# Optimization experiments

Hardware: AMD Instinct MI355X
Metric: run time of the kernel (lower is better)

Reference implementation:

```python
import jax, jax.numpy as jnp
import numpy as np

DIM = 128; NH = 4; WS = 7; SS = 3
ZP, HP, WP = 14, 56, 56
NMLP = 512; EPS = 1e-5
N = WS ** 3  # tokens per window (343)


def _ln(x, g, b):
    m = x.mean(-1, keepdims=True)
    v = x.var(-1, keepdims=True)
    return (x - m) / jnp.sqrt(v + EPS) * g + b


def _rel_index():
    # static relative-position index for a cubic (WS,WS,WS) window
    c = np.stack(np.meshgrid(np.arange(WS), np.arange(WS), np.arange(WS), indexing='ij')).reshape(3, -1)
    rel = (c[:, :, None] - c[:, None, :]).transpose(1, 2, 0) + (WS - 1)
    rel[..., 0] *= (2 * WS - 1) ** 2
    rel[..., 1] *= (2 * WS - 1)
    return rel.sum(-1).reshape(-1)  # [N*N]


def _attn_mask():
    # static shifted-window attention mask, [nW, N, N]
    img = np.zeros((ZP, HP, WP), np.float32)
    cnt = 0
    sl = (slice(0, -WS), slice(-WS, -SS), slice(-SS, None))
    for z in sl:
        for h in sl:
            for w in sl:
                img[z, h, w] = cnt
                cnt += 1
    m = img.reshape(ZP // WS, WS, HP // WS, WS, WP // WS, WS)
    m = m.transpose(0, 2, 4, 1, 3, 5).reshape(-1, N)
    d = m[:, None, :] - m[:, :, None]
    return np.where(d != 0, np.float32(-100.0), np.float32(0.0))


_REL_IDX = jnp.asarray(_rel_index())
_MASK = jnp.asarray(_attn_mask())


def setup_inputs() -> dict:
    key = jax.random.key(0)
    ks = jax.random.split(key, 8)
    return {
        'x': jax.random.normal(ks[0], (2, ZP, HP, WP, DIM), jnp.float32),
        'norm1_g': jnp.ones((DIM,), jnp.float32),
        'norm1_b': jnp.zeros((DIM,), jnp.float32),
        'qkv_w': jax.random.normal(ks[1], (DIM, 3 * DIM), jnp.float32) * 0.02,
        'qkv_b': jnp.zeros((3 * DIM,), jnp.float32),
        'rel_table': jax.random.normal(ks[2], ((2 * WS - 1) ** 3, NH), jnp.float32) * 0.02,
        'proj_w': jax.random.normal(ks[3], (DIM, DIM), jnp.float32) * 0.02,
        'proj_b': jnp.zeros((DIM,), jnp.float32),
        'norm2_g': jnp.ones((DIM,), jnp.float32),
        'norm2_b': jnp.zeros((DIM,), jnp.float32),
        'fc1_w': jax.random.normal(ks[4], (DIM, NMLP), jnp.float32) * 0.02,
        'fc1_b': jnp.zeros((NMLP,), jnp.float32),
        'fc2_w': jax.random.normal(ks[5], (NMLP, DIM), jnp.float32) * 0.02,
        'fc2_b': jnp.zeros((DIM,), jnp.float32),
    }


def reference(x, norm1_g, norm1_b, qkv_w, qkv_b, rel_table, proj_w, proj_b,
              norm2_g, norm2_b, fc1_w, fc1_b, fc2_w, fc2_b):
    B, Z, H, W, C = x.shape
    hd = C // NH
    scale = hd ** -0.5
    shortcut = x
    xn = _ln(x, norm1_g, norm1_b)
    # cyclic shift
    xs = jnp.roll(xn, (-SS, -SS, -SS), axis=(1, 2, 3))
    # window partition -> [B*nW, N, C]
    xw = xs.reshape(B, Z // WS, WS, H // WS, WS, W // WS, WS, C)
    xw = xw.transpose(0, 1, 3, 5, 2, 4, 6, 7).reshape(-1, N, C)
    qkv = (xw @ qkv_w + qkv_b).reshape(-1, N, 3, NH, hd).transpose(2, 0, 3, 1, 4)
    q, k, v = qkv[0], qkv[1], qkv[2]  # [Bn, NH, N, hd]
    attn = jnp.einsum('bhnd,bhmd->bhnm', q * scale, k)
    bias = rel_table[_REL_IDX].reshape(N, N, NH).transpose(2, 0, 1)  # [NH, N, N]
    attn = attn + bias[None]
    nW = _MASK.shape[0]
    attn = attn.reshape(B, nW, NH, N, N) + _MASK[None, :, None]
    attn = jax.nn.softmax(attn.reshape(-1, NH, N, N), axis=-1)
    out = jnp.einsum('bhnm,bhmd->bhnd', attn, v)
    out = out.transpose(0, 2, 1, 3).reshape(-1, N, C)
    out = out @ proj_w + proj_b
    # window reverse -> [B, Z, H, W, C]
    out = out.reshape(B, Z // WS, H // WS, W // WS, WS, WS, WS, C)
    out = out.transpose(0, 1, 4, 2, 5, 3, 6, 7).reshape(B, Z, H, W, C)
    out = jnp.roll(out, (SS, SS, SS), axis=(1, 2, 3))
    x1 = shortcut + out
    y = _ln(x1, norm2_g, norm2_b)
    y = jax.nn.gelu(y @ fc1_w + fc1_b, approximate=False) @ fc2_w + fc2_b
    return x1 + y
```

## Files before the change

kernel.cpp:

```cpp
#include <hip/hip_runtime.h>


typedef __attribute__((ext_vector_type(8))) _Float16 half8;
typedef __attribute__((ext_vector_type(4))) _Float16 half4;
typedef __attribute__((ext_vector_type(4))) float floatx4;

#define DEV static __device__ __forceinline__

DEV floatx4 MFMA(half8 a, half8 b, floatx4 c) {
  return __builtin_amdgcn_mfma_f32_16x16x32_f16(a, b, c, 0, 0, 0);
}

DEV float gelu_f(float v) {
  return v / (1.f + __expf(-1.702f * v));
}

DEV void stage_load(half8 pf[8], const _Float16* src, int rst, int tid) {
#pragma unroll
  for (int it = 0; it < 8; ++it) {
    int e = it * 256 + tid;
    int row = e >> 4, seg = e & 15;
    pf[it] = *(const half8*)&src[(size_t)row * rst + seg * 8];
  }
}
DEV void stage_store(_Float16* wb, const half8 pf[8], int tid) {
#pragma unroll
  for (int it = 0; it < 8; ++it) {
    int e = it * 256 + tid;
    int row = e >> 4, seg = e & 15;
    *(half8*)&wb[row * 136 + seg * 8] = pf[it];
  }
}
DEV void stage_tile(_Float16* wb, const _Float16* src, int rst, int tid) {
  half8 pf[8];
  stage_load(pf, src, rst, tid);
  stage_store(wb, pf, tid);
}

__global__ __launch_bounds__(256) void k_prep(
    const float* __restrict__ rel, _Float16* __restrict__ biasH,
    const float* __restrict__ w1, const float* __restrict__ w2,
    const float* __restrict__ wq, const float* __restrict__ wp,
    _Float16* __restrict__ w1h, _Float16* __restrict__ w2h,
    _Float16* __restrict__ wqh, _Float16* __restrict__ wph) {
  int gid = blockIdx.x * 256 + threadIdx.x;
  if (gid < 495616) {
    int reg = gid & 3, ml = (gid >> 2) & 15;
    int t = gid >> 6;
    int rb = t % 88; t /= 88;
    int nt = t % 22; int h = t / 22;
    int row = rb * 4 + reg, col = nt * 16 + ml;
    float val = -30000.f;
    if (row < 343 && col < 343) {
      int lzi = row / 49, ri = row - lzi * 49, lhi = ri / 7, lwi = ri - lhi * 7;
      int lzj = col / 49, rj = col - lzj * 49, lhj = rj / 7, lwj = rj - lhj * 7;
      int idx = (lzi - lzj + 6) * 169 + (lhi - lhj + 6) * 13 + (lwi - lwj + 6);
      val = rel[idx * 4 + h];
    }
    biasH[gid] = (_Float16)val;
    return;
  }
  int i = gid - 495616;
  if (i < 65536) {
    int n = i >> 7, k = i & 127;
    w1h[i] = (_Float16)w1[k * 512 + n];
  } else if (i < 131072) {
    int j = i - 65536; int n = j >> 9, k = j & 511;
    w2h[j] = (_Float16)w2[k * 128 + n];
  } else if (i < 180224) {
    int j = i - 131072; int n = j >> 7, k = j & 127;
    wqh[j] = (_Float16)wq[k * 384 + n];
  } else if (i < 196608) {
    int j = i - 180224; int n = j >> 7, k = j & 127;
    wph[j] = (_Float16)wp[k * 128 + n];
  }
}

__global__ __launch_bounds__(256) void k_ln_qkv(
    const float* __restrict__ x, const float* __restrict__ g1,
    const float* __restrict__ b1, const _Float16* __restrict__ wqh,
    const float* __restrict__ bq, _Float16* __restrict__ qkv) {
  __shared__ __align__(16) _Float16 wb[128 * 136];
  const int tid = threadIdx.x, lane = tid & 63, wid = tid >> 6;
  const int ml = lane & 15, quad = lane >> 4;
  const int task = blockIdx.x * 4 + wid;
  const int w = task / 11, pr = task - (task / 11) * 11;
  const int b_ = w >> 7, r = w & 127;
  const int wz = r >> 6, wh = (r >> 3) & 7, ww = r & 7;

  half8 a0[4], a1[4];
#pragma unroll
  for (int hf = 0; hf < 2; ++hf) {
    int t = pr * 32 + hf * 16 + ml; if (t > 342) t = 342;
    int lz = t / 49, rr = t - lz * 49, lh = rr / 7, lw = rr - lh * 7;
    int oz = wz * 7 + lz + 3; if (oz >= 14) oz -= 14;
    int oh = wh * 7 + lh + 3; if (oh >= 56) oh -= 56;
    int ow = ww * 7 + lw + 3; if (ow >= 56) ow -= 56;
    const float* xp = x + ((((b_ * 14 + oz) * 56 + oh) * 56 + ow) << 7);
    float xv[32];
    float s = 0.f, ss = 0.f;
#pragma unroll
    for (int ks = 0; ks < 4; ++ks) {
      float4 p0 = *(const float4*)(xp + ks * 32 + quad * 8);
      float4 p1 = *(const float4*)(xp + ks * 32 + quad * 8 + 4);
      xv[ks * 8 + 0] = p0.x; xv[ks * 8 + 1] = p0.y; xv[ks * 8 + 2] = p0.z; xv[ks * 8 + 3] = p0.w;
      xv[ks * 8 + 4] = p1.x; xv[ks * 8 + 5] = p1.y; xv[ks * 8 + 6] = p1.z; xv[ks * 8 + 7] = p1.w;
      s += (p0.x + p0.y) + (p0.z + p0.w) + (p1.x + p1.y) + (p1.z + p1.w);
      ss += (p0.x * p0.x + p0.y * p0.y) + (p0.z * p0.z + p0.w * p0.w) +
            (p1.x * p1.x + p1.y * p1.y) + (p1.z * p1.z + p1.w * p1.w);
    }
    s += __shfl_xor(s, 16); s += __shfl_xor(s, 32);
    ss += __shfl_xor(ss, 16); ss += __shfl_xor(ss, 32);
    float mean = s * 0.0078125f;
    float rstd = rsqrtf(ss * 0.0078125f - mean * mean + 1e-5f);
#pragma unroll
    for (int ks = 0; ks < 4; ++ks) {
      int k0 = ks * 32 + quad * 8;
      float4 gg0 = *(const float4*)(g1 + k0), gg1 = *(const float4*)(g1 + k0 + 4);
      float4 bb0 = *(const float4*)(b1 + k0), bb1 = *(const float4*)(b1 + k0 + 4);
      half8 a;
      a[0] = (_Float16)((xv[ks * 8 + 0] - mean) * rstd * gg0.x + bb0.x);
      a[1] = (_Float16)((xv[ks * 8 + 1] - mean) * rstd * gg0.y + bb0.y);
      a[2] = (_Float16)((xv[ks * 8 + 2] - mean) * rstd * gg0.z + bb0.z);
      a[3] = (_Float16)((xv[ks * 8 + 3] - mean) * rstd * gg0.w + bb0.w);
      a[4] = (_Float16)((xv[ks * 8 + 4] - mean) * rstd * gg1.x + bb1.x);
      a[5] = (_Float16)((xv[ks * 8 + 5] - mean) * rstd * gg1.y + bb1.y);
      a[6] = (_Float16)((xv[ks * 8 + 6] - mean) * rstd * gg1.z + bb1.z);
      a[7] = (_Float16)((xv[ks * 8 + 7] - mean) * rstd * gg1.w + bb1.w);
      if (hf == 0) a0[ks] = a; else a1[ks] = a;
    }
  }

  for (int c = 0; c < 3; ++c) {
    __syncthreads();
    stage_tile(wb, wqh + (size_t)c * 128 * 128, 128, tid);
    __syncthreads();
    for (int ntl = 0; ntl < 8; ++ntl) {
      floatx4 acc0 = {0.f, 0.f, 0.f, 0.f}, acc1 = {0.f, 0.f, 0.f, 0.f};
#pragma unroll
      for (int ks = 0; ks < 4; ++ks) {
        half8 bb = *(const half8*)&wb[(ntl * 16 + ml) * 136 + ks * 32 + quad * 8];
        acc0 = MFMA(a0[ks], bb, acc0);
        acc1 = MFMA(a1[ks], bb, acc1);
      }
      const int col = c * 128 + ntl * 16 + ml;
      const float qb = bq[col];
#pragma unroll
      for (int reg = 0; reg < 4; ++reg) {
        int t0 = pr * 32 + quad * 4 + reg;
        if (t0 < 343) qkv[((size_t)w * 343 + t0) * 384 + col] = (_Float16)(acc0[reg] + qb);
        int t1 = t0 + 16;
        if (t1 < 343) qkv[((size_t)w * 343 + t1) * 384 + col] = (_Float16)(acc1[reg] + qb);
      }
    }
  }
}

__global__ __launch_bounds__(512)
__attribute__((amdgpu_waves_per_eu(2, 2)))
void k_attn(const _Float16* __restrict__ qkv,
            const _Float16* __restrict__ biasH,
            _Float16* __restrict__ aout) {
  __shared__ __align__(16) _Float16 kl[352 * 40];
  __shared__ __align__(16) _Float16 vt[32 * 360];
  __shared__ __align__(16) _Float16 P[8][16 * 360];
  __shared__ float sums[8][16];
  __shared__ unsigned char region[352];
  const int tid = threadIdx.x;
  const int w = blockIdx.x >> 2, head = blockIdx.x & 3;
  const int r = w & 127;
  const int wz = r >> 6, wh = (r >> 3) & 7, ww = r & 7;
  const bool fz = (wz == 1), fh = (wh == 7), fw = (ww == 7);

  for (int t = tid; t < 352; t += 512) {
    int rg = 255;
    if (t < 343) {
      int lz = t / 49, rr = t - lz * 49, lh = rr / 7, lw = rr - lh * 7;
      int rz = fz ? (lz < 4 ? 1 : 2) : 0;
      int rh2 = fh ? (lh < 4 ? 1 : 2) : 0;
      int rw2 = fw ? (lw < 4 ? 1 : 2) : 0;
      rg = rz * 9 + rh2 * 3 + rw2;
    }
    region[t] = (unsigned char)rg;
  }
  const _Float16* qkvw = qkv + (size_t)w * 343 * 384;
  for (int e = tid; e < 352 * 4; e += 512) {
    int t = e >> 2, d8 = (e & 3) * 8;
    half8 v;
    if (t < 343) {
      v = *(const half8*)&qkvw[t * 384 + 128 + head * 32 + d8];
    } else {
#pragma unroll
      for (int j = 0; j < 8; ++j) v[j] = (_Float16)0.f;
    }
    *(half8*)&kl[t * 40 + d8] = v;
  }
  for (int e = tid; e < 343 * 4; e += 512) {
    int t = e >> 2, d8 = (e & 3) * 8;
    half8 v = *(const half8*)&qkvw[t * 384 + 256 + head * 32 + d8];
#pragma unroll
    for (int j = 0; j < 8; ++j) vt[(d8 + j) * 360 + t] = v[j];
  }
  for (int e = tid; e < 9 * 32; e += 512) {
    int t = 343 + (e >> 5), d = e & 31;
    vt[d * 360 + t] = (_Float16)0.f;
  }
  __syncthreads();

  const int lane = tid & 63, wid = tid >> 6;
  const int ml = lane & 15, quad = lane >> 4;
  _Float16* Pw = &P[wid][0];
  const float scale = 0.17677669529663687f;

  for (int rt = wid; rt < 22; rt += 8) {
    const int row0 = rt * 16;
    int qrow = row0 + ml; if (qrow > 342) qrow = 342;
    half8 aq = *(const half8*)&qkvw[qrow * 384 + head * 32 + quad * 8];
    floatx4 S[22];
#pragma unroll
    for (int nt = 0; nt < 22; ++nt) {
      half8 bk = *(const half8*)&kl[(nt * 16 + ml) * 40 + quad * 8];
      S[nt] = MFMA(aq, bk, (floatx4){0.f, 0.f, 0.f, 0.f});
    }
    int rrow[4];
#pragma unroll
    for (int reg = 0; reg < 4; ++reg) rrow[reg] = region[row0 + quad * 4 + reg];
    const int rb = rt * 4 + quad;
    float sm[4] = {0.f, 0.f, 0.f, 0.f};
#pragma unroll
    for (int nt = 0; nt < 22; ++nt) {
      half4 b4 = *(const half4*)&biasH[((((head * 22 + nt) * 88 + rb) << 4) + ml) * 4];
      int rc = region[nt * 16 + ml];
#pragma unroll
      for (int reg = 0; reg < 4; ++reg) {
        float v = fmaf(S[nt][reg], scale, (float)b4[reg]);
        if (rc != rrow[reg]) v = -30000.f;
        float e = __expf(v);
        sm[reg] += e;
        Pw[(quad * 4 + reg) * 360 + nt * 16 + ml] = (_Float16)e;
      }
    }
#pragma unroll
    for (int d = 1; d < 16; d <<= 1)
#pragma unroll
      for (int reg = 0; reg < 4; ++reg) sm[reg] += __shfl_xor(sm[reg], d, 16);
    if (ml == 0) {
#pragma unroll
      for (int reg = 0; reg < 4; ++reg) sums[wid][quad * 4 + reg] = sm[reg];
    }
    floatx4 o0 = {0.f, 0.f, 0.f, 0.f}, o1 = {0.f, 0.f, 0.f, 0.f};
#pragma unroll
    for (int ks = 0; ks < 11; ++ks) {
      half8 bp = *(const half8*)&Pw[ml * 360 + ks * 32 + quad * 8];
      half8 a0 = *(const half8*)&vt[ml * 360 + ks * 32 + quad * 8];
      half8 a1 = *(const half8*)&vt[(16 + ml) * 360 + ks * 32 + quad * 8];
      o0 = MFMA(a0, bp, o0);
      o1 = MFMA(a1, bp, o1);
    }
    const int orow = row0 + ml;
    if (orow < 343) {
      float inv = 1.f / sums[wid][ml];
      _Float16* op = aout + ((size_t)w * 343 + orow) * 128 + head * 32;
      half4 s0, s1;
#pragma unroll
      for (int reg = 0; reg < 4; ++reg) {
        s0[reg] = (_Float16)(o0[reg] * inv);
        s1[reg] = (_Float16)(o1[reg] * inv);
      }
      *(half4*)&op[quad * 4] = s0;
      *(half4*)&op[16 + quad * 4] = s1;
    }
  }
}

__global__ __launch_bounds__(256)
__attribute__((amdgpu_waves_per_eu(2, 2)))
void k_pm(
    const _Float16* __restrict__ aout, const _Float16* __restrict__ wph,
    const float* __restrict__ bp, const float* __restrict__ x,
    const float* __restrict__ g2, const float* __restrict__ nb2,
    const _Float16* __restrict__ w1h, const float* __restrict__ bfc1,
    const _Float16* __restrict__ w2h, const float* __restrict__ bfc2,
    float* __restrict__ out) {
  __shared__ __align__(16) _Float16 hc[4][32 * 136];
  __shared__ __align__(16) _Float16 wb[128 * 136];
  const int tid = threadIdx.x, lane = tid & 63, wid = tid >> 6;
  const int ml = lane & 15, quad = lane >> 4;
  const int task = blockIdx.x * 4 + wid;
  const int w = task / 11, pr = task - (task / 11) * 11;
  const int b_ = w >> 7, r = w & 127;
  const int wz = r >> 6, wh = (r >> 3) & 7, ww = r & 7;
  const _Float16* ap = aout + (size_t)w * 343 * 128;
  _Float16* hw = &hc[wid][0];

  half8 pf[8];
  stage_load(pf, wph, 128, tid);

  int ra = pr * 32 + ml; if (ra > 342) ra = 342;
  int rbm = pr * 32 + 16 + ml; if (rbm > 342) rbm = 342;
  half8 a0[4], a1[4];
#pragma unroll
  for (int ks = 0; ks < 4; ++ks) {
    a0[ks] = *(const half8*)&ap[ra * 128 + ks * 32 + quad * 8];
    a1[ks] = *(const half8*)&ap[rbm * 128 + ks * 32 + quad * 8];
  }
  int tok[2][4];
#pragma unroll
  for (int mt = 0; mt < 2; ++mt) {
#pragma unroll
    for (int reg = 0; reg < 4; ++reg) {
      int t = pr * 32 + mt * 16 + quad * 4 + reg;
      if (t < 343) {
        int lz = t / 49, rr = t - lz * 49, lh = rr / 7, lw = rr - lh * 7;
        int oz = wz * 7 + lz + 3; if (oz >= 14) oz -= 14;
        int oh = wh * 7 + lh + 3; if (oh >= 56) oh -= 56;
        int ow = ww * 7 + lw + 3; if (ow >= 56) ow -= 56;
        tok[mt][reg] = ((b_ * 14 + oz) * 56 + oh) * 56 + ow;
      } else {
        tok[mt][reg] = -1;
      }
    }
  }
  stage_store(wb, pf, tid);
  __syncthreads();
  stage_load(pf, w1h, 128, tid);

  floatx4 px[8][2];
  for (int nt = 0; nt < 8; ++nt) {
    floatx4 acc0 = {0.f, 0.f, 0.f, 0.f}, acc1 = {0.f, 0.f, 0.f, 0.f};
#pragma unroll
    for (int ks = 0; ks < 4; ++ks) {
      half8 bb = *(const half8*)&wb[(nt * 16 + ml) * 136 + ks * 32 + quad * 8];
      acc0 = MFMA(a0[ks], bb, acc0);
      acc1 = MFMA(a1[ks], bb, acc1);
    }
    const int col = nt * 16 + ml;
    const float pb = bp[col];
#pragma unroll
    for (int reg = 0; reg < 4; ++reg) {
      float xr0 = (tok[0][reg] >= 0) ? x[tok[0][reg] * 128 + col] : 0.f;
      float xr1 = (tok[1][reg] >= 0) ? x[tok[1][reg] * 128 + col] : 0.f;
      px[nt][0][reg] = acc0[reg] + pb + xr0;
      px[nt][1][reg] = acc1[reg] + pb + xr1;
    }
  }

  float mean[2][4], rstd[2][4];
#pragma unroll
  for (int mt = 0; mt < 2; ++mt) {
#pragma unroll
    for (int reg = 0; reg < 4; ++reg) {
      float s = 0.f, ss = 0.f;
#pragma unroll
      for (int nt = 0; nt < 8; ++nt) {
        float v = px[nt][mt][reg];
        s += v; ss += v * v;
      }
#pragma unroll
      for (int d = 1; d < 16; d <<= 1) {
        s += __shfl_xor(s, d, 16);
        ss += __shfl_xor(ss, d, 16);
      }
      float m = s * 0.0078125f;
      mean[mt][reg] = m;
      rstd[mt][reg] = rsqrtf(ss * 0.0078125f - m * m + 1e-5f);
    }
  }

  for (int nt = 0; nt < 8; ++nt) {
    const int col = nt * 16 + ml;
    const float gg = g2[col], bb = nb2[col];
#pragma unroll
    for (int mt = 0; mt < 2; ++mt)
#pragma unroll
      for (int reg = 0; reg < 4; ++reg)
        hw[(mt * 16 + quad * 4 + reg) * 136 + col] =
            (_Float16)((px[nt][mt][reg] - mean[mt][reg]) * rstd[mt][reg] * gg + bb);
  }
  half8 ay[2][4];
#pragma unroll
  for (int mt = 0; mt < 2; ++mt)
#pragma unroll
    for (int ks = 0; ks < 4; ++ks)
      ay[mt][ks] = *(const half8*)&hw[(mt * 16 + ml) * 136 + ks * 32 + quad * 8];

  floatx4 acc2[8][2];
#pragma unroll
  for (int nt = 0; nt < 8; ++nt)
#pragma unroll
    for (int mt = 0; mt < 2; ++mt) acc2[nt][mt] = (floatx4){0.f, 0.f, 0.f, 0.f};

  for (int ch = 0; ch < 4; ++ch) {
    __syncthreads();
    stage_store(wb, pf, tid);
    __syncthreads();
    stage_load(pf, w2h + (size_t)ch * 128, 512, tid);
    for (int nt = 0; nt < 8; ++nt) {
      floatx4 f0 = {0.f, 0.f, 0.f, 0.f}, f1 = {0.f, 0.f, 0.f, 0.f};
#pragma unroll
      for (int ks = 0; ks < 4; ++ks) {
        half8 bb = *(const half8*)&wb[(nt * 16 + ml) * 136 + ks * 32 + quad * 8];
        f0 = MFMA(ay[0][ks], bb, f0);
        f1 = MFMA(ay[1][ks], bb, f1);
      }
      const int col = nt * 16 + ml;
      const float fb = bfc1[ch * 128 + col];
#pragma unroll
      for (int reg = 0; reg < 4; ++reg) {
        hw[(quad * 4 + reg) * 136 + col] = (_Float16)gelu_f(f0[reg] + fb);
        hw[(16 + quad * 4 + reg) * 136 + col] = (_Float16)gelu_f(f1[reg] + fb);
      }
    }
    __syncthreads();
    stage_store(wb, pf, tid);
    __syncthreads();
    if (ch < 3) stage_load(pf, w1h + (size_t)(ch + 1) * 128 * 128, 128, tid);
#pragma unroll
    for (int ks = 0; ks < 4; ++ks) {
      half8 A0 = *(const half8*)&hw[ml * 136 + ks * 32 + quad * 8];
      half8 A1 = *(const half8*)&hw[(16 + ml) * 136 + ks * 32 + quad * 8];
#pragma unroll
      for (int nt = 0; nt < 8; ++nt) {
        half8 bb = *(const half8*)&wb[(nt * 16 + ml) * 136 + ks * 32 + quad * 8];
        acc2[nt][0] = MFMA(A0, bb, acc2[nt][0]);
        acc2[nt][1] = MFMA(A1, bb, acc2[nt][1]);
      }
    }
  }

  for (int nt = 0; nt < 8; ++nt) {
    const int col = nt * 16 + ml;
    const float fb = bfc2[col];
#pragma unroll
    for (int mt = 0; mt < 2; ++mt)
#pragma unroll
      for (int reg = 0; reg < 4; ++reg) {
        if (tok[mt][reg] >= 0)
          out[tok[mt][reg] * 128 + col] = px[nt][mt][reg] + acc2[nt][mt][reg] + fb;
      }
  }
}

extern "C" void kernel_launch(void* const* d_in, const int* in_sizes, int n_in,
                              void* d_out, int out_size, void* d_ws, size_t ws_size,
                              hipStream_t stream) {
  (void)in_sizes; (void)n_in; (void)out_size; (void)ws_size;
  const float* x   = (const float*)d_in[0];
  const float* g1  = (const float*)d_in[1];
  const float* b1  = (const float*)d_in[2];
  const float* wq  = (const float*)d_in[3];
  const float* bq  = (const float*)d_in[4];
  const float* rel = (const float*)d_in[5];
  const float* wp  = (const float*)d_in[6];
  const float* bp  = (const float*)d_in[7];
  const float* g2  = (const float*)d_in[8];
  const float* b2_ = (const float*)d_in[9];
  const float* w1  = (const float*)d_in[10];
  const float* bf1 = (const float*)d_in[11];
  const float* w2  = (const float*)d_in[12];
  const float* bf2 = (const float*)d_in[13];

  char* ws = (char*)d_ws;
  _Float16* qkv   = (_Float16*)(ws);
  _Float16* aout  = (_Float16*)(ws + 67436544);
  _Float16* biasH = (_Float16*)(ws + 89915392);
  _Float16* w1h   = (_Float16*)(ws + 91897856);
  _Float16* w2h   = (_Float16*)(ws + 92028928);
  _Float16* wqh   = (_Float16*)(ws + 92160000);
  _Float16* wph   = (_Float16*)(ws + 92258304);
  float*    out   = (float*)d_out;

  hipLaunchKernelGGL(k_prep,   dim3(2704), dim3(256), 0, stream,
                     rel, biasH, w1, w2, wq, wp, w1h, w2h, wqh, wph);
  hipLaunchKernelGGL(k_ln_qkv, dim3(704),  dim3(256), 0, stream, x, g1, b1, wqh, bq, qkv);
  hipLaunchKernelGGL(k_attn,   dim3(1024), dim3(512), 0, stream, qkv, biasH, aout);
  hipLaunchKernelGGL(k_pm,     dim3(704),  dim3(256), 0, stream,
                     aout, wph, bp, x, g2, b2_, w1h, bf1, w2h, bf2, out);
}
```

Measured before the change: 335.4 us.

## Process two heads per attention block with prefetched K/V; coalesce MLP output stores

The attention kernel now handles two heads per block, so half as many blocks are launched. The next head's K and V are prefetched into registers while the current head computes, then swapped into shared memory behind barriers. This spreads the region-setup cost over two heads and hides global load latency, at the cost of extra registers and fewer blocks. Separately, the fused MLP kernel stages its output tile through shared memory so each row is written as contiguous float4 stores instead of scattered per-column scalar stores.

```diff
diff --git a/kernel.cpp b/kernel.cpp
--- a/kernel.cpp
+++ b/kernel.cpp
@@ -167,7 +167,7 @@
   __shared__ float sums[8][16];
   __shared__ unsigned char region[352];
   const int tid = threadIdx.x;
-  const int w = blockIdx.x >> 2, head = blockIdx.x & 3;
+  const int w = blockIdx.x >> 1, hp = (blockIdx.x & 1) * 2;
   const int r = w & 127;
   const int wz = r >> 6, wh = (r >> 3) & 7, ww = r & 7;
   const bool fz = (wz == 1), fh = (wh == 7), fw = (ww == 7);
@@ -188,7 +188,7 @@
     int t = e >> 2, d8 = (e & 3) * 8;
     half8 v;
     if (t < 343) {
-      v = *(const half8*)&qkvw[t * 384 + 128 + head * 32 + d8];
+      v = *(const half8*)&qkvw[t * 384 + 128 + hp * 32 + d8];
     } else {
 #pragma unroll
       for (int j = 0; j < 8; ++j) v[j] = (_Float16)0.f;
@@ -197,7 +197,7 @@
   }
   for (int e = tid; e < 343 * 4; e += 512) {
     int t = e >> 2, d8 = (e & 3) * 8;
-    half8 v = *(const half8*)&qkvw[t * 384 + 256 + head * 32 + d8];
+    half8 v = *(const half8*)&qkvw[t * 384 + 256 + hp * 32 + d8];
 #pragma unroll
     for (int j = 0; j < 8; ++j) vt[(d8 + j) * 360 + t] = v[j];
   }
@@ -212,63 +212,96 @@
   _Float16* Pw = &P[wid][0];
   const float scale = 0.17677669529663687f;
 
-  for (int rt = wid; rt < 22; rt += 8) {
-    const int row0 = rt * 16;
-    int qrow = row0 + ml; if (qrow > 342) qrow = 342;
-    half8 aq = *(const half8*)&qkvw[qrow * 384 + head * 32 + quad * 8];
-    floatx4 S[22];
-#pragma unroll
-    for (int nt = 0; nt < 22; ++nt) {
-      half8 bk = *(const half8*)&kl[(nt * 16 + ml) * 40 + quad * 8];
-      S[nt] = MFMA(aq, bk, (floatx4){0.f, 0.f, 0.f, 0.f});
-    }
-    int rrow[4];
-#pragma unroll
-    for (int reg = 0; reg < 4; ++reg) rrow[reg] = region[row0 + quad * 4 + reg];
-    const int rb = rt * 4 + quad;
-    float sm[4] = {0.f, 0.f, 0.f, 0.f};
-#pragma unroll
-    for (int nt = 0; nt < 22; ++nt) {
-      half4 b4 = *(const half4*)&biasH[((((head * 22 + nt) * 88 + rb) << 4) + ml) * 4];
-      int rc = region[nt * 16 + ml];
-#pragma unroll
-      for (int reg = 0; reg < 4; ++reg) {
-        float v = fmaf(S[nt][reg], scale, (float)b4[reg]);
-        if (rc != rrow[reg]) v = -30000.f;
-        float e = __expf(v);
-        sm[reg] += e;
-        Pw[(quad * 4 + reg) * 360 + nt * 16 + ml] = (_Float16)e;
-      }
-    }
-#pragma unroll
-    for (int d = 1; d < 16; d <<= 1)
-#pragma unroll
-      for (int reg = 0; reg < 4; ++reg) sm[reg] += __shfl_xor(sm[reg], d, 16);
-    if (ml == 0) {
-#pragma unroll
-      for (int reg = 0; reg < 4; ++reg) sums[wid][quad * 4 + reg] = sm[reg];
-    }
-    floatx4 o0 = {0.f, 0.f, 0.f, 0.f}, o1 = {0.f, 0.f, 0.f, 0.f};
-#pragma unroll
-    for (int ks = 0; ks < 11; ++ks) {
-      half8 bp = *(const half8*)&Pw[ml * 360 + ks * 32 + quad * 8];
-      half8 a0 = *(const half8*)&vt[ml * 360 + ks * 32 + quad * 8];
-      half8 a1 = *(const half8*)&vt[(16 + ml) * 360 + ks * 32 + quad * 8];
-      o0 = MFMA(a0, bp, o0);
-      o1 = MFMA(a1, bp, o1);
-    }
-    const int orow = row0 + ml;
-    if (orow < 343) {
-      float inv = 1.f / sums[wid][ml];
-      _Float16* op = aout + ((size_t)w * 343 + orow) * 128 + head * 32;
-      half4 s0, s1;
-#pragma unroll
-      for (int reg = 0; reg < 4; ++reg) {
-        s0[reg] = (_Float16)(o0[reg] * inv);
-        s1[reg] = (_Float16)(o1[reg] * inv);
-      }
-      *(half4*)&op[quad * 4] = s0;
-      *(half4*)&op[16 + quad * 4] = s1;
+  half8 pk[3], pv[3];
+  for (int hh = 0; hh < 2; ++hh) {
+    const int head = hp + hh;
+    if (hh == 0) {
+#pragma unroll
+      for (int it = 0; it < 3; ++it) {
+        int e = it * 512 + tid;
+        half8 z;
+#pragma unroll
+        for (int j = 0; j < 8; ++j) z[j] = (_Float16)0.f;
+        pk[it] = z; pv[it] = z;
+        int t = e >> 2, d8 = (e & 3) * 8;
+        if (e < 1408 && t < 343)
+          pk[it] = *(const half8*)&qkvw[t * 384 + 128 + (hp + 1) * 32 + d8];
+        if (e < 1372)
+          pv[it] = *(const half8*)&qkvw[t * 384 + 256 + (hp + 1) * 32 + d8];
+      }
+    }
+    for (int rt = wid; rt < 22; rt += 8) {
+      const int row0 = rt * 16;
+      int qrow = row0 + ml; if (qrow > 342) qrow = 342;
+      half8 aq = *(const half8*)&qkvw[qrow * 384 + head * 32 + quad * 8];
+      floatx4 S[22];
+#pragma unroll
+      for (int nt = 0; nt < 22; ++nt) {
+        half8 bk = *(const half8*)&kl[(nt * 16 + ml) * 40 + quad * 8];
+        S[nt] = MFMA(aq, bk, (floatx4){0.f, 0.f, 0.f, 0.f});
+      }
+      int rrow[4];
+#pragma unroll
+      for (int reg = 0; reg < 4; ++reg) rrow[reg] = region[row0 + quad * 4 + reg];
+      const int rb = rt * 4 + quad;
+      float sm[4] = {0.f, 0.f, 0.f, 0.f};
+#pragma unroll
+      for (int nt = 0; nt < 22; ++nt) {
+        half4 b4 = *(const half4*)&biasH[((((head * 22 + nt) * 88 + rb) << 4) + ml) * 4];
+        int rc = region[nt * 16 + ml];
+#pragma unroll
+        for (int reg = 0; reg < 4; ++reg) {
+          float v = fmaf(S[nt][reg], scale, (float)b4[reg]);
+          if (rc != rrow[reg]) v = -30000.f;
+          float e = __expf(v);
+          sm[reg] += e;
+          Pw[(quad * 4 + reg) * 360 + nt * 16 + ml] = (_Float16)e;
+        }
+      }
+#pragma unroll
+      for (int d = 1; d < 16; d <<= 1)
+#pragma unroll
+        for (int reg = 0; reg < 4; ++reg) sm[reg] += __shfl_xor(sm[reg], d, 16);
+      if (ml == 0) {
+#pragma unroll
+        for (int reg = 0; reg < 4; ++reg) sums[wid][quad * 4 + reg] = sm[reg];
+      }
+      floatx4 o0 = {0.f, 0.f, 0.f, 0.f}, o1 = {0.f, 0.f, 0.f, 0.f};
+#pragma unroll
+      for (int ks = 0; ks < 11; ++ks) {
+        half8 bp = *(const half8*)&Pw[ml * 360 + ks * 32 + quad * 8];
+        half8 a0 = *(const half8*)&vt[ml * 360 + ks * 32 + quad * 8];
+        half8 a1 = *(const half8*)&vt[(16 + ml) * 360 + ks * 32 + quad * 8];
+        o0 = MFMA(a0, bp, o0);
+        o1 = MFMA(a1, bp, o1);
+      }
+      const int orow = row0 + ml;
+      if (orow < 343) {
+        float inv = 1.f / sums[wid][ml];
+        _Float16* op = aout + ((size_t)w * 343 + orow) * 128 + head * 32;
+        half4 s0, s1;
+#pragma unroll
+        for (int reg = 0; reg < 4; ++reg) {
+          s0[reg] = (_Float16)(o0[reg] * inv);
+          s1[reg] = (_Float16)(o1[reg] * inv);
+        }
+        *(half4*)&op[quad * 4] = s0;
+        *(half4*)&op[16 + quad * 4] = s1;
+      }
+    }
+    if (hh == 0) {
+      __syncthreads();
+#pragma unroll
+      for (int it = 0; it < 3; ++it) {
+        int e = it * 512 + tid;
+        int t = e >> 2, d8 = (e & 3) * 8;
+        if (e < 1408) *(half8*)&kl[t * 40 + d8] = pk[it];
+        if (e < 1372) {
+#pragma unroll
+          for (int j = 0; j < 8; ++j) vt[(d8 + j) * 360 + t] = pv[it][j];
+        }
+      }
+      __syncthreads();
     }
   }
 }
@@ -284,6 +317,7 @@
     float* __restrict__ out) {
   __shared__ __align__(16) _Float16 hc[4][32 * 136];
   __shared__ __align__(16) _Float16 wb[128 * 136];
+  __shared__ int tokl[4][32];
   const int tid = threadIdx.x, lane = tid & 63, wid = tid >> 6;
   const int ml = lane & 15, quad = lane >> 4;
   const int task = blockIdx.x * 4 + wid;
@@ -292,6 +326,7 @@
   const int wz = r >> 6, wh = (r >> 3) & 7, ww = r & 7;
   const _Float16* ap = aout + (size_t)w * 343 * 128;
   _Float16* hw = &hc[wid][0];
+  float* hwf = (float*)hw;
 
   half8 pf[8];
   stage_load(pf, wph, 128, tid);
@@ -319,6 +354,7 @@
       } else {
         tok[mt][reg] = -1;
       }
+      if (ml == 0) tokl[wid][mt * 16 + quad * 4 + reg] = tok[mt][reg];
     }
   }
   stage_store(wb, pf, tid);
@@ -428,16 +464,23 @@
     }
   }
 
-  for (int nt = 0; nt < 8; ++nt) {
-    const int col = nt * 16 + ml;
-    const float fb = bfc2[col];
-#pragma unroll
-    for (int mt = 0; mt < 2; ++mt)
-#pragma unroll
-      for (int reg = 0; reg < 4; ++reg) {
-        if (tok[mt][reg] >= 0)
-          out[tok[mt][reg] * 128 + col] = px[nt][mt][reg] + acc2[nt][mt][reg] + fb;
-      }
+  const int sr = lane >> 5, seg = lane & 31;
+#pragma unroll
+  for (int mt = 0; mt < 2; ++mt) {
+    for (int nt = 0; nt < 8; ++nt) {
+      const int col = nt * 16 + ml;
+      const float fb = bfc2[col];
+#pragma unroll
+      for (int reg = 0; reg < 4; ++reg)
+        hwf[(quad * 4 + reg) * 132 + col] = px[nt][mt][reg] + acc2[nt][mt][reg] + fb;
+    }
+#pragma unroll
+    for (int ir = 0; ir < 8; ++ir) {
+      int lr = ir * 2 + sr;
+      int t = tokl[wid][mt * 16 + lr];
+      if (t >= 0)
+        *(float4*)&out[(size_t)t * 128 + seg * 4] = *(const float4*)&hwf[lr * 132 + seg * 4];
+    }
   }
 }
 
@@ -473,7 +516,7 @@
   hipLaunchKernelGGL(k_prep,   dim3(2704), dim3(256), 0, stream,
                      rel, biasH, w1, w2, wq, wp, w1h, w2h, wqh, wph);
   hipLaunchKernelGGL(k_ln_qkv, dim3(704),  dim3(256), 0, stream, x, g1, b1, wqh, bq, qkv);
-  hipLaunchKernelGGL(k_attn,   dim3(1024), dim3(512), 0, stream, qkv, biasH, aout);
+  hipLaunchKernelGGL(k_attn,   dim3(512),  dim3(512), 0, stream, qkv, biasH, aout);
   hipLaunchKernelGGL(k_pm,     dim3(704),  dim3(256), 0, stream,
                      aout, wph, bp, x, g2, b2_, w1h, bf1, w2h, bf2, out);
 }
```

Measured after the change: 360.8 us. 7.6% more time.
